# Kernel optimization log

Hardware: AMD Instinct MI355X
Metric: run time of the kernel (lower is better)

## Reference

```python
import jax, jax.numpy as jnp
import numpy as np

TOP_K = 2


def setup_inputs() -> dict:
    key = jax.random.key(0)
    ks = jax.random.split(key, 5)
    B, S, H, E, F = 4, 1024, 1024, 16, 4096
    scale = 0.02
    return {
        "input_tensor": jax.random.normal(ks[0], (B, S, H), dtype=jnp.float32),
        "Wg": scale * jax.random.normal(ks[1], (H, E), dtype=jnp.float32),
        "bg": jnp.zeros((E,), dtype=jnp.float32),
        "W1": scale * jax.random.normal(ks[2], (E, H, F), dtype=jnp.float32),
        "b1": jnp.zeros((E, F), dtype=jnp.float32),
        "W2": scale * jax.random.normal(ks[3], (E, F, H), dtype=jnp.float32),
        "b2": jnp.zeros((E, H), dtype=jnp.float32),
    }


def reference(input_tensor, Wg, bg, W1, b1, W2, b2):
    # Faithful to DualOutputMoE.forward_first_pass: the per-(b,s,k) Python loop
    # plus _weighted_sum collapses ALL token expert outputs into a single
    # [1,1,H] vector normalized by the total routing weight (= B*S).
    B, S, H = input_tensor.shape
    T = B * S
    E = Wg.shape[1]
    x = input_tensor.reshape(T, H)

    routing_scores = x @ Wg + bg                    # [T, E] (raw gate logits)
    top_v, top_i = jax.lax.top_k(routing_scores, TOP_K)
    top_w = jax.nn.softmax(top_v, axis=-1)          # per-token top-k weights

    # combine[t, e] = sum_k top_w[t, k] * 1[top_i[t, k] == e]
    combine = jnp.zeros((T, E), x.dtype).at[jnp.arange(T)[:, None], top_i].add(top_w)
    total_weight = top_w.sum()                      # matches python sum of .item()s

    def expert_step(acc, params):
        w1, bb1, w2, bb2, c = params                # c: [T] combine weights for this expert
        y = jax.nn.gelu(x @ w1 + bb1, approximate=False) @ w2 + bb2  # [T, H]
        return acc + c @ y, None

    acc0 = jnp.zeros((H,), x.dtype)
    acc, _ = jax.lax.scan(expert_step, acc0, (W1, b1, W2, b2, combine.T))
    first_output = (acc / total_weight).reshape(1, 1, H)
    return first_output
```

## Files before the change

kernel.cpp:

```cpp
#include <hip/hip_runtime.h>
#include <hip/hip_bf16.h>
#include <math.h>

typedef __bf16 bf16_t;
typedef __bf16 bf16x4 __attribute__((ext_vector_type(4)));
typedef __bf16 bf16x8 __attribute__((ext_vector_type(8)));
typedef float  f32x4  __attribute__((ext_vector_type(4)));

#define T_TOK 4096
#define H_DIM 1024
#define E_NUM 16
#define F_DIM 4096
#define CH_MAX 16

#define WS_E0     0
#define WS_E1     16384
#define WS_W0     32768
#define WS_W1     49152
#define WS_COUNTS 65536
#define WS_SUMW   65664
#define WS_XOFF   65792
#define WS_LIDX   131072
#define WS_LW     393216
#define WS_GPART  655360
#define WS_G      4849664
#define WS_P2     5111808
#define WS_XE     7208960

#define AS_GLOBAL(p) ((const __attribute__((address_space(1))) void*)(p))
#define AS_LDS(p)    ((__attribute__((address_space(3))) void*)(p))

__global__ __launch_bounds__(64) void k_route(const float* __restrict__ x,
    const float* __restrict__ Wg, const float* __restrict__ bg,
    int* __restrict__ e0, int* __restrict__ e1,
    float* __restrict__ w0, float* __restrict__ w1)
{
    const int t = blockIdx.x;
    const int lane = threadIdx.x;
    const float* xr = x + (size_t)t * H_DIM;

    float s[E_NUM];
#pragma unroll
    for (int e = 0; e < E_NUM; ++e) s[e] = 0.f;

#pragma unroll
    for (int i = 0; i < 16; ++i) {
        const int h = i * 64 + lane;
        const float xv = xr[h];
        const float4* wr = (const float4*)(Wg + (size_t)h * E_NUM);
        float4 q0 = wr[0], q1 = wr[1], q2 = wr[2], q3 = wr[3];
        s[0] += xv*q0.x;  s[1] += xv*q0.y;  s[2] += xv*q0.z;  s[3] += xv*q0.w;
        s[4] += xv*q1.x;  s[5] += xv*q1.y;  s[6] += xv*q1.z;  s[7] += xv*q1.w;
        s[8] += xv*q2.x;  s[9] += xv*q2.y;  s[10]+= xv*q2.z;  s[11]+= xv*q2.w;
        s[12]+= xv*q3.x;  s[13]+= xv*q3.y;  s[14]+= xv*q3.z;  s[15]+= xv*q3.w;
    }
#pragma unroll
    for (int off = 32; off >= 1; off >>= 1) {
#pragma unroll
        for (int e = 0; e < E_NUM; ++e) s[e] += __shfl_xor(s[e], off);
    }
    if (lane == 0) {
#pragma unroll
        for (int e = 0; e < E_NUM; ++e) s[e] += bg[e];
        float b1v = -3e38f; int i1 = 0;
#pragma unroll
        for (int e = 0; e < E_NUM; ++e) { if (s[e] > b1v) { b1v = s[e]; i1 = e; } }
        float b2v = -3e38f; int i2 = 0;
#pragma unroll
        for (int e = 0; e < E_NUM; ++e) { if (e != i1 && s[e] > b2v) { b2v = s[e]; i2 = e; } }
        const float ex  = expf(b2v - b1v);
        const float inv = 1.f / (1.f + ex);
        e0[t] = i1; e1[t] = i2;
        w0[t] = inv; w1[t] = ex * inv;
    }
}

__global__ __launch_bounds__(64) void k_lists(const int* __restrict__ e0, const int* __restrict__ e1,
    const float* __restrict__ w0, const float* __restrict__ w1,
    int* __restrict__ lidx, float* __restrict__ lw,
    int* __restrict__ counts, float* __restrict__ sumw)
{
    const int e = blockIdx.x;
    const int lane = threadIdx.x;
    int cnt = 0; float sw = 0.f;
    for (int base = 0; base < T_TOK; base += 64) {
        const int t = base + lane;
        const bool m0 = (e0[t] == e);
        const bool m1 = (e1[t] == e);
        const bool m  = m0 | m1;
        const unsigned long long bal = __ballot(m);
        const int pos = cnt + __popcll(bal & ((1ull << lane) - 1ull));
        if (m) {
            const float w = m0 ? w0[t] : w1[t];
            lidx[e * T_TOK + pos] = t;
            lw[e * T_TOK + pos]   = w;
            sw += w;
        }
        cnt += __popcll(bal);
    }
#pragma unroll
    for (int off = 32; off >= 1; off >>= 1) sw += __shfl_xor(sw, off);
    if (lane == 0) { counts[e] = cnt; sumw[e] = sw; }
}

__global__ void k_scan(const int* __restrict__ counts, int* __restrict__ xoff) {
    if (threadIdx.x == 0) {
        int o = 0;
        for (int e = 0; e < E_NUM; ++e) { xoff[e] = o; o += (counts[e] + 255) & ~255; }
    }
}

__global__ __launch_bounds__(256) void k_gather(const float* __restrict__ x,
    const int* __restrict__ lidx, const int* __restrict__ counts,
    const int* __restrict__ xoff, bf16_t* __restrict__ Xe)
{
    const int chunk = blockIdx.x, e = blockIdx.y;
    const int cnt = counts[e];
    const int start = chunk * 256;
    if (chunk && start >= cnt) return;
    const int tid = threadIdx.x;
    const size_t rbase = (size_t)xoff[e] + start;

    for (int it = 0; it < 128; ++it) {
        const int task = it * 256 + tid;
        const int rl   = task >> 7;
        const int sc   = task & 127;
        const int row  = start + rl;
        bf16x8 v8 = {};
        if (row < cnt) {
            const int tok = lidx[e * T_TOK + row];
            const int l   = (sc & 7) ^ (rl & 7);
            const int k   = (sc >> 3) * 64 + l * 8;
            const float4 a = *(const float4*)(x + (size_t)tok * H_DIM + k);
            const float4 b = *(const float4*)(x + (size_t)tok * H_DIM + k + 4);
            v8[0]=(bf16_t)a.x; v8[1]=(bf16_t)a.y; v8[2]=(bf16_t)a.z; v8[3]=(bf16_t)a.w;
            v8[4]=(bf16_t)b.x; v8[5]=(bf16_t)b.y; v8[6]=(bf16_t)b.z; v8[7]=(bf16_t)b.w;
        }
        *(bf16x8*)(Xe + (rbase + rl) * H_DIM + sc * 8) = v8;
    }
}

__global__ __launch_bounds__(256, 2) void k_expert(
    const float* __restrict__ W1, const float* __restrict__ b1,
    const bf16_t* __restrict__ Xe, const float* __restrict__ lw,
    const int* __restrict__ counts, const int* __restrict__ xoff,
    float* __restrict__ gpart)
{
    const int ftile = blockIdx.x;
    const int chunk = blockIdx.y;
    const int e     = blockIdx.z;
    const int cnt   = counts[e];
    const int start = chunk * 256;
    if (chunk && start >= cnt) return;

    __shared__ __align__(16) bf16_t Alds[256 * 64];
    __shared__ __align__(16) bf16_t Blds[64 * 72];
    __shared__ float w_s[256];
    __shared__ float b1_s[64];
    __shared__ float gred[4][64];

    const int tid  = threadIdx.x;
    const int lane = tid & 63;
    const int wid  = tid >> 6;
    const int lr   = lane & 15;
    const int lg   = lane >> 4;

    {
        const int r = start + tid;
        w_s[tid] = (r < cnt) ? lw[e * T_TOK + r] : 0.f;
        if (tid < 64) b1_s[tid] = b1[(size_t)e * F_DIM + ftile * 64 + tid];
    }

    f32x4 acc[4][4];
#pragma unroll
    for (int i = 0; i < 4; ++i)
#pragma unroll
        for (int j = 0; j < 4; ++j)
#pragma unroll
            for (int q = 0; q < 4; ++q) acc[i][j][q] = 0.f;

    const bf16_t* Asrc = Xe + ((size_t)xoff[e] + start) * H_DIM;
    const float* W1p = W1 + (size_t)e * H_DIM * F_DIM + (size_t)ftile * 64 + lane;

    for (int k0 = 0; k0 < H_DIM; k0 += 64) {
#pragma unroll
        for (int p = 0; p < 8; ++p) {
            const int seg = wid * 8 + p;
            const int r   = seg * 8 + (lane >> 3);
            const int c   = lane & 7;
            const bf16_t* src = Asrc + (size_t)r * H_DIM + k0 + c * 8;
            __builtin_amdgcn_global_load_lds(AS_GLOBAL(src),
                AS_LDS((char*)Alds + seg * 1024), 16, 0, 0);
        }
        {
            const float* wp = W1p + (size_t)(k0 + wid * 16) * F_DIM;
            float bv[16];
#pragma unroll
            for (int j = 0; j < 16; ++j) bv[j] = wp[(size_t)j * F_DIM];
            bf16x8 pk0, pk1;
#pragma unroll
            for (int q = 0; q < 8; ++q) { pk0[q] = (bf16_t)bv[q]; pk1[q] = (bf16_t)bv[8 + q]; }
            bf16_t* bdst = &Blds[lane * 72 + wid * 16];
            *(bf16x8*)bdst       = pk0;
            *(bf16x8*)(bdst + 8) = pk1;
        }
        __syncthreads();

#pragma unroll
        for (int kh = 0; kh < 2; ++kh) {
            bf16x8 af[4], bfr[4];
#pragma unroll
            for (int mf = 0; mf < 4; ++mf) {
                const int r = wid * 64 + mf * 16 + lr;
                const int eoff = (kh * 32 + lg * 8) ^ ((r & 7) * 8);
                af[mf] = *(const bf16x8*)&Alds[r * 64 + eoff];
            }
#pragma unroll
            for (int nf = 0; nf < 4; ++nf)
                bfr[nf] = *(const bf16x8*)&Blds[(nf * 16 + lr) * 72 + kh * 32 + lg * 8];
#pragma unroll
            for (int mf = 0; mf < 4; ++mf)
#pragma unroll
                for (int nf = 0; nf < 4; ++nf)
                    acc[mf][nf] = __builtin_amdgcn_mfma_f32_16x16x32_bf16(af[mf], bfr[nf], acc[mf][nf], 0, 0, 0);
        }
        __syncthreads();
    }

    float gcol[4] = {0.f, 0.f, 0.f, 0.f};
#pragma unroll
    for (int nf = 0; nf < 4; ++nf) {
        const float bb = b1_s[nf * 16 + lr];
#pragma unroll
        for (int mf = 0; mf < 4; ++mf) {
#pragma unroll
            for (int i = 0; i < 4; ++i) {
                const int row = wid * 64 + mf * 16 + lg * 4 + i;
                const float h  = acc[mf][nf][i] + bb;
                const float gl = 0.5f * h * (1.f + erff(h * 0.70710678118654752f));
                gcol[nf] += w_s[row] * gl;
            }
        }
    }
#pragma unroll
    for (int nf = 0; nf < 4; ++nf) {
        gcol[nf] += __shfl_xor(gcol[nf], 16);
        gcol[nf] += __shfl_xor(gcol[nf], 32);
    }
    if (lane < 16) {
#pragma unroll
        for (int nf = 0; nf < 4; ++nf) gred[wid][nf * 16 + lane] = gcol[nf];
    }
    __syncthreads();
    if (tid < 64) {
        const float sum = gred[0][tid] + gred[1][tid] + gred[2][tid] + gred[3][tid];
        gpart[(size_t)(e * CH_MAX + chunk) * F_DIM + ftile * 64 + tid] = sum;
    }
}

__global__ __launch_bounds__(256) void k_redg(const float* __restrict__ gpart,
    const int* __restrict__ counts, float* __restrict__ g)
{
    const int e = blockIdx.y;
    const int f = blockIdx.x * 256 + threadIdx.x;
    const int nch = (counts[e] + 255) >> 8;
    float s = 0.f;
    for (int c = 0; c < nch; ++c)
        s += gpart[(size_t)(e * CH_MAX + c) * F_DIM + f];
    g[(size_t)e * F_DIM + f] = s;
}

__global__ __launch_bounds__(256) void k_out1(const float* __restrict__ g,
    const float* __restrict__ W2, float* __restrict__ p2)
{
    const int fc = blockIdx.x;
    const int e  = blockIdx.y;
    const int tid = threadIdx.x;
    __shared__ float gs[128];
    if (tid < 128) gs[tid] = g[(size_t)e * F_DIM + fc * 128 + tid];
    __syncthreads();
    const float* W2p = W2 + (size_t)e * F_DIM * H_DIM + (size_t)fc * 128 * H_DIM;
    float ax = 0.f, ay = 0.f, az = 0.f, aw = 0.f;
#pragma unroll 4
    for (int f = 0; f < 128; ++f) {
        const float gv = gs[f];
        const float4 wv = *(const float4*)(W2p + (size_t)f * H_DIM + tid * 4);
        ax += gv * wv.x; ay += gv * wv.y; az += gv * wv.z; aw += gv * wv.w;
    }
    float4 st; st.x = ax; st.y = ay; st.z = az; st.w = aw;
    *(float4*)(p2 + (size_t)(e * 32 + fc) * H_DIM + tid * 4) = st;
}

__global__ __launch_bounds__(256) void k_out2(const float* __restrict__ p2,
    const float* __restrict__ sumw, const float* __restrict__ b2, float* __restrict__ out)
{
    const int tid = threadIdx.x;
    const int hh  = tid & 31;
    const int seg = tid >> 5;
    const int h   = blockIdx.x * 32 + hh;
    float s = 0.f;
    for (int j = 0; j < 64; ++j)
        s += p2[(size_t)(seg * 64 + j) * H_DIM + h];
    __shared__ float red[8][33];
    red[seg][hh] = s;
    __syncthreads();
    if (tid < 32) {
        const int h2 = blockIdx.x * 32 + tid;
        float tot = 0.f;
#pragma unroll
        for (int q = 0; q < 8; ++q) tot += red[q][tid];
        float tw = 0.f, bias = 0.f;
#pragma unroll
        for (int e = 0; e < E_NUM; ++e) { tw += sumw[e]; bias += sumw[e] * b2[e * H_DIM + h2]; }
        out[h2] = (tot + bias) / tw;
    }
}

extern "C" void kernel_launch(void* const* d_in, const int* in_sizes, int n_in,
                              void* d_out, int out_size, void* d_ws, size_t ws_size,
                              hipStream_t stream) {
    const float* x  = (const float*)d_in[0];
    const float* Wg = (const float*)d_in[1];
    const float* bg = (const float*)d_in[2];
    const float* W1 = (const float*)d_in[3];
    const float* b1 = (const float*)d_in[4];
    const float* W2 = (const float*)d_in[5];
    const float* b2 = (const float*)d_in[6];
    float* out = (float*)d_out;

    char* ws = (char*)d_ws;
    int*    e0     = (int*)(ws + WS_E0);
    int*    e1     = (int*)(ws + WS_E1);
    float*  w0     = (float*)(ws + WS_W0);
    float*  w1     = (float*)(ws + WS_W1);
    int*    counts = (int*)(ws + WS_COUNTS);
    float*  sumw   = (float*)(ws + WS_SUMW);
    int*    xoff   = (int*)(ws + WS_XOFF);
    int*    lidx   = (int*)(ws + WS_LIDX);
    float*  lw     = (float*)(ws + WS_LW);
    float*  gpart  = (float*)(ws + WS_GPART);
    float*  g      = (float*)(ws + WS_G);
    float*  p2     = (float*)(ws + WS_P2);
    bf16_t* Xe     = (bf16_t*)(ws + WS_XE);

    k_route<<<T_TOK, 64, 0, stream>>>(x, Wg, bg, e0, e1, w0, w1);
    k_lists<<<E_NUM, 64, 0, stream>>>(e0, e1, w0, w1, lidx, lw, counts, sumw);
    k_scan<<<1, 64, 0, stream>>>(counts, xoff);
    k_gather<<<dim3(CH_MAX, E_NUM), 256, 0, stream>>>(x, lidx, counts, xoff, Xe);
    k_expert<<<dim3(F_DIM / 64, CH_MAX, E_NUM), 256, 0, stream>>>(W1, b1, Xe, lw, counts, xoff, gpart);
    k_redg<<<dim3(F_DIM / 256, E_NUM), 256, 0, stream>>>(gpart, counts, g);
    k_out1<<<dim3(32, E_NUM), 256, 0, stream>>>(g, W2, p2);
    k_out2<<<32, 256, 0, stream>>>(p2, sumw, b2, out);
}
```

Measured before the change: 383.8 us.

## Double-buffer expert GEMM tiles and halve token chunk size

The expert GEMM now double-buffers its A and B LDS tiles, prefetching the next K-slice while MFMAs run on the current one. The token chunk shrinks from 256 to 128 rows, with a 2x2 wave layout and occupancy raised to 3 blocks per SM. The gather is split across four blocks per chunk, and the W2 reduction loop is unrolled further. Smaller chunks mean each W1 tile is fetched by more blocks, which may raise global or L2 traffic on the fp32 weights. The p2 buffer now reuses the gpart workspace region.

```diff
diff --git a/kernel.cpp b/kernel.cpp
--- a/kernel.cpp
+++ b/kernel.cpp
@@ -11,7 +11,8 @@
 #define H_DIM 1024
 #define E_NUM 16
 #define F_DIM 4096
-#define CH_MAX 16
+#define CH_ROWS 128
+#define CH_MAX  32
 
 #define WS_E0     0
 #define WS_E1     16384
@@ -23,9 +24,9 @@
 #define WS_LIDX   131072
 #define WS_LW     393216
 #define WS_GPART  655360
-#define WS_G      4849664
-#define WS_P2     5111808
-#define WS_XE     7208960
+#define WS_P2     655360
+#define WS_G      9043968
+#define WS_XE     9306112
 
 #define AS_GLOBAL(p) ((const __attribute__((address_space(1))) void*)(p))
 #define AS_LDS(p)    ((__attribute__((address_space(3))) void*)(p))
@@ -106,7 +107,7 @@
 __global__ void k_scan(const int* __restrict__ counts, int* __restrict__ xoff) {
     if (threadIdx.x == 0) {
         int o = 0;
-        for (int e = 0; e < E_NUM; ++e) { xoff[e] = o; o += (counts[e] + 255) & ~255; }
+        for (int e = 0; e < E_NUM; ++e) { xoff[e] = o; o += (counts[e] + CH_ROWS - 1) & ~(CH_ROWS - 1); }
     }
 }
 
@@ -114,14 +115,16 @@
     const int* __restrict__ lidx, const int* __restrict__ counts,
     const int* __restrict__ xoff, bf16_t* __restrict__ Xe)
 {
-    const int chunk = blockIdx.x, e = blockIdx.y;
+    const int chunk = blockIdx.x >> 2;
+    const int part  = blockIdx.x & 3;
+    const int e = blockIdx.y;
     const int cnt = counts[e];
-    const int start = chunk * 256;
+    const int start = chunk * CH_ROWS;
     if (chunk && start >= cnt) return;
     const int tid = threadIdx.x;
     const size_t rbase = (size_t)xoff[e] + start;
 
-    for (int it = 0; it < 128; ++it) {
+    for (int it = part * 16; it < part * 16 + 16; ++it) {
         const int task = it * 256 + tid;
         const int rl   = task >> 7;
         const int sc   = task & 127;
@@ -140,7 +143,7 @@
     }
 }
 
-__global__ __launch_bounds__(256, 2) void k_expert(
+__global__ __launch_bounds__(256, 3) void k_expert(
     const float* __restrict__ W1, const float* __restrict__ b1,
     const bf16_t* __restrict__ Xe, const float* __restrict__ lw,
     const int* __restrict__ counts, const int* __restrict__ xoff,
@@ -150,92 +153,122 @@
     const int chunk = blockIdx.y;
     const int e     = blockIdx.z;
     const int cnt   = counts[e];
-    const int start = chunk * 256;
+    const int start = chunk * CH_ROWS;
     if (chunk && start >= cnt) return;
 
-    __shared__ __align__(16) bf16_t Alds[256 * 64];
-    __shared__ __align__(16) bf16_t Blds[64 * 72];
-    __shared__ float w_s[256];
+    __shared__ __align__(16) bf16_t Alds[2][CH_ROWS * 64];
+    __shared__ __align__(16) bf16_t Blds[2][64 * 72];
+    __shared__ float w_s[CH_ROWS];
     __shared__ float b1_s[64];
-    __shared__ float gred[4][64];
+    __shared__ float gred[2][64];
 
     const int tid  = threadIdx.x;
     const int lane = tid & 63;
     const int wid  = tid >> 6;
+    const int wm   = wid & 1;
+    const int wn   = wid >> 1;
     const int lr   = lane & 15;
     const int lg   = lane >> 4;
 
-    {
+    if (tid < CH_ROWS) {
         const int r = start + tid;
         w_s[tid] = (r < cnt) ? lw[e * T_TOK + r] : 0.f;
-        if (tid < 64) b1_s[tid] = b1[(size_t)e * F_DIM + ftile * 64 + tid];
-    }
-
-    f32x4 acc[4][4];
+    } else if (tid < CH_ROWS + 64) {
+        b1_s[tid - CH_ROWS] = b1[(size_t)e * F_DIM + ftile * 64 + (tid - CH_ROWS)];
+    }
+
+    f32x4 acc[4][2];
 #pragma unroll
     for (int i = 0; i < 4; ++i)
 #pragma unroll
-        for (int j = 0; j < 4; ++j)
+        for (int j = 0; j < 2; ++j)
 #pragma unroll
             for (int q = 0; q < 4; ++q) acc[i][j][q] = 0.f;
 
     const bf16_t* Asrc = Xe + ((size_t)xoff[e] + start) * H_DIM;
-    const float* W1p = W1 + (size_t)e * H_DIM * F_DIM + (size_t)ftile * 64 + lane;
-
-    for (int k0 = 0; k0 < H_DIM; k0 += 64) {
-#pragma unroll
-        for (int p = 0; p < 8; ++p) {
-            const int seg = wid * 8 + p;
-            const int r   = seg * 8 + (lane >> 3);
-            const int c   = lane & 7;
-            const bf16_t* src = Asrc + (size_t)r * H_DIM + k0 + c * 8;
+    const float*  W1p  = W1 + (size_t)e * H_DIM * F_DIM + (size_t)ftile * 64 + lane;
+
+    const int arow = (wid * 4) * 8 + (lane >> 3);
+    const int acol = lane & 7;
+
+    float bv[16];
+
+    {
+        const float* wp = W1p + (size_t)(wid * 16) * F_DIM;
+#pragma unroll
+        for (int j = 0; j < 16; ++j) bv[j] = wp[(size_t)j * F_DIM];
+#pragma unroll
+        for (int p = 0; p < 4; ++p) {
+            const int seg = wid * 4 + p;
+            const bf16_t* src = Asrc + (size_t)(seg * 8 + (lane >> 3)) * H_DIM + acol * 8;
             __builtin_amdgcn_global_load_lds(AS_GLOBAL(src),
-                AS_LDS((char*)Alds + seg * 1024), 16, 0, 0);
-        }
-        {
+                AS_LDS((char*)&Alds[0][0] + seg * 1024), 16, 0, 0);
+        }
+        bf16x8 pk0, pk1;
+#pragma unroll
+        for (int q = 0; q < 8; ++q) { pk0[q] = (bf16_t)bv[q]; pk1[q] = (bf16_t)bv[8 + q]; }
+        bf16_t* bdst = &Blds[0][lane * 72 + wid * 16];
+        *(bf16x8*)bdst       = pk0;
+        *(bf16x8*)(bdst + 8) = pk1;
+    }
+    __syncthreads();
+
+    int cur = 0;
+    for (int t = 0; t < H_DIM / 64; ++t) {
+        const int nxt = cur ^ 1;
+        const bool more = (t + 1) < (H_DIM / 64);
+        if (more) {
+            const int k0 = (t + 1) * 64;
             const float* wp = W1p + (size_t)(k0 + wid * 16) * F_DIM;
-            float bv[16];
 #pragma unroll
             for (int j = 0; j < 16; ++j) bv[j] = wp[(size_t)j * F_DIM];
+#pragma unroll
+            for (int p = 0; p < 4; ++p) {
+                const int seg = wid * 4 + p;
+                const bf16_t* src = Asrc + (size_t)(seg * 8 + (lane >> 3)) * H_DIM + k0 + acol * 8;
+                __builtin_amdgcn_global_load_lds(AS_GLOBAL(src),
+                    AS_LDS((char*)&Alds[nxt][0] + seg * 1024), 16, 0, 0);
+            }
+        }
+#pragma unroll
+        for (int kh = 0; kh < 2; ++kh) {
+            bf16x8 af[4], bfr[2];
+#pragma unroll
+            for (int mf = 0; mf < 4; ++mf) {
+                const int r = wm * 64 + mf * 16 + lr;
+                const int eoff = (kh * 32 + lg * 8) ^ ((r & 7) * 8);
+                af[mf] = *(const bf16x8*)&Alds[cur][r * 64 + eoff];
+            }
+#pragma unroll
+            for (int nf = 0; nf < 2; ++nf)
+                bfr[nf] = *(const bf16x8*)&Blds[cur][(wn * 32 + nf * 16 + lr) * 72 + kh * 32 + lg * 8];
+#pragma unroll
+            for (int mf = 0; mf < 4; ++mf)
+#pragma unroll
+                for (int nf = 0; nf < 2; ++nf)
+                    acc[mf][nf] = __builtin_amdgcn_mfma_f32_16x16x32_bf16(af[mf], bfr[nf], acc[mf][nf], 0, 0, 0);
+        }
+        if (more) {
             bf16x8 pk0, pk1;
 #pragma unroll
             for (int q = 0; q < 8; ++q) { pk0[q] = (bf16_t)bv[q]; pk1[q] = (bf16_t)bv[8 + q]; }
-            bf16_t* bdst = &Blds[lane * 72 + wid * 16];
+            bf16_t* bdst = &Blds[nxt][lane * 72 + wid * 16];
             *(bf16x8*)bdst       = pk0;
             *(bf16x8*)(bdst + 8) = pk1;
         }
         __syncthreads();
-
-#pragma unroll
-        for (int kh = 0; kh < 2; ++kh) {
-            bf16x8 af[4], bfr[4];
-#pragma unroll
-            for (int mf = 0; mf < 4; ++mf) {
-                const int r = wid * 64 + mf * 16 + lr;
-                const int eoff = (kh * 32 + lg * 8) ^ ((r & 7) * 8);
-                af[mf] = *(const bf16x8*)&Alds[r * 64 + eoff];
-            }
-#pragma unroll
-            for (int nf = 0; nf < 4; ++nf)
-                bfr[nf] = *(const bf16x8*)&Blds[(nf * 16 + lr) * 72 + kh * 32 + lg * 8];
-#pragma unroll
-            for (int mf = 0; mf < 4; ++mf)
-#pragma unroll
-                for (int nf = 0; nf < 4; ++nf)
-                    acc[mf][nf] = __builtin_amdgcn_mfma_f32_16x16x32_bf16(af[mf], bfr[nf], acc[mf][nf], 0, 0, 0);
-        }
-        __syncthreads();
-    }
-
-    float gcol[4] = {0.f, 0.f, 0.f, 0.f};
-#pragma unroll
-    for (int nf = 0; nf < 4; ++nf) {
-        const float bb = b1_s[nf * 16 + lr];
+        cur = nxt;
+    }
+
+    float gcol[2] = {0.f, 0.f};
+#pragma unroll
+    for (int nf = 0; nf < 2; ++nf) {
+        const float bb = b1_s[wn * 32 + nf * 16 + lr];
 #pragma unroll
         for (int mf = 0; mf < 4; ++mf) {
 #pragma unroll
             for (int i = 0; i < 4; ++i) {
-                const int row = wid * 64 + mf * 16 + lg * 4 + i;
+                const int row = wm * 64 + mf * 16 + lg * 4 + i;
                 const float h  = acc[mf][nf][i] + bb;
                 const float gl = 0.5f * h * (1.f + erff(h * 0.70710678118654752f));
                 gcol[nf] += w_s[row] * gl;
@@ -243,17 +276,17 @@
         }
     }
 #pragma unroll
-    for (int nf = 0; nf < 4; ++nf) {
+    for (int nf = 0; nf < 2; ++nf) {
         gcol[nf] += __shfl_xor(gcol[nf], 16);
         gcol[nf] += __shfl_xor(gcol[nf], 32);
     }
     if (lane < 16) {
 #pragma unroll
-        for (int nf = 0; nf < 4; ++nf) gred[wid][nf * 16 + lane] = gcol[nf];
+        for (int nf = 0; nf < 2; ++nf) gred[wm][wn * 32 + nf * 16 + lane] = gcol[nf];
     }
     __syncthreads();
     if (tid < 64) {
-        const float sum = gred[0][tid] + gred[1][tid] + gred[2][tid] + gred[3][tid];
+        const float sum = gred[0][tid] + gred[1][tid];
         gpart[(size_t)(e * CH_MAX + chunk) * F_DIM + ftile * 64 + tid] = sum;
     }
 }
@@ -263,7 +296,7 @@
 {
     const int e = blockIdx.y;
     const int f = blockIdx.x * 256 + threadIdx.x;
-    const int nch = (counts[e] + 255) >> 8;
+    const int nch = (counts[e] + CH_ROWS - 1) / CH_ROWS;
     float s = 0.f;
     for (int c = 0; c < nch; ++c)
         s += gpart[(size_t)(e * CH_MAX + c) * F_DIM + f];
@@ -281,7 +314,7 @@
     __syncthreads();
     const float* W2p = W2 + (size_t)e * F_DIM * H_DIM + (size_t)fc * 128 * H_DIM;
     float ax = 0.f, ay = 0.f, az = 0.f, aw = 0.f;
-#pragma unroll 4
+#pragma unroll 8
     for (int f = 0; f < 128; ++f) {
         const float gv = gs[f];
         const float4 wv = *(const float4*)(W2p + (size_t)f * H_DIM + tid * 4);
@@ -346,7 +379,7 @@
     k_route<<<T_TOK, 64, 0, stream>>>(x, Wg, bg, e0, e1, w0, w1);
     k_lists<<<E_NUM, 64, 0, stream>>>(e0, e1, w0, w1, lidx, lw, counts, sumw);
     k_scan<<<1, 64, 0, stream>>>(counts, xoff);
-    k_gather<<<dim3(CH_MAX, E_NUM), 256, 0, stream>>>(x, lidx, counts, xoff, Xe);
+    k_gather<<<dim3(CH_MAX * 4, E_NUM), 256, 0, stream>>>(x, lidx, counts, xoff, Xe);
     k_expert<<<dim3(F_DIM / 64, CH_MAX, E_NUM), 256, 0, stream>>>(W1, b1, Xe, lw, counts, xoff, gpart);
     k_redg<<<dim3(F_DIM / 256, E_NUM), 256, 0, stream>>>(gpart, counts, g);
     k_out1<<<dim3(32, E_NUM), 256, 0, stream>>>(g, W2, p2);
```

Measured after the change: 313.5 us. -18.3%, faster.
